# Performance work log

Hardware: AMD Instinct MI355X
Metric: run time of the kernel (lower is better)

## Reference

```python
import jax, jax.numpy as jnp
import numpy as np

# Hyperparameters matching init_kwargs
IN_CH = 64
OUT_CH = 128
KERNEL = (3, 3)
STRIDE = (1, 1)
PADDING = 'SAME'
K_ORDER = 3          # spline order
G_INTERVALS = 3      # grid intervals
GRID_MIN, GRID_MAX = -1.0, 1.0
N_BASIS = G_INTERVALS + K_ORDER  # basis functions per input = 6
PATCH_DIM = IN_CH * KERNEL[0] * KERNEL[1]  # 576


def _grid():
    # Extended uniform knot vector: G + 2k + 1 knots
    h = (GRID_MAX - GRID_MIN) / G_INTERVALS
    return jnp.arange(-K_ORDER, G_INTERVALS + K_ORDER + 1, dtype=jnp.float32) * h + GRID_MIN


def _b_splines(x):
    # x: [N, n_in] -> bases: [N, n_in, G + k]
    grid = _grid()  # [G + 2k + 1]
    xe = x[..., None]  # [N, n_in, 1]
    bases = ((xe >= grid[:-1]) & (xe < grid[1:])).astype(x.dtype)  # order-0, [N, n_in, G+2k]
    for p in range(1, K_ORDER + 1):
        left = (xe - grid[: -(p + 1)]) / (grid[p:-1] - grid[: -(p + 1)]) * bases[..., :-1]
        right = (grid[p + 1:] - xe) / (grid[p + 1:] - grid[1:-p]) * bases[..., 1:]
        bases = left + right
    return bases  # [N, n_in, G + k]


def setup_inputs() -> dict:
    key = jax.random.key(0)
    k0, k1, k2, k3 = jax.random.split(key, 4)
    x = jax.random.normal(k0, (8, 64, 64, IN_CH), dtype=jnp.float32)
    base_w = jax.random.normal(k1, (OUT_CH, PATCH_DIM), dtype=jnp.float32) * 0.05
    spline_w = jax.random.normal(k2, (OUT_CH, PATCH_DIM, N_BASIS), dtype=jnp.float32) * 0.05
    bias = jax.random.normal(k3, (OUT_CH,), dtype=jnp.float32) * 0.05
    return {'x': x, 'base_w': base_w, 'spline_w': spline_w, 'bias': bias}


def reference(x, base_w, spline_w, bias):
    batch = x.shape[0]
    dn = ('NHWC', 'HWIO', 'NHWC')
    patches = jax.lax.conv_general_dilated_patches(
        lhs=x, filter_shape=KERNEL, window_strides=STRIDE, padding=PADDING,
        dimension_numbers=dn)  # [B, H, W, patch_dim]
    out_spatial = patches.shape[1:-1]
    p = patches.reshape(-1, PATCH_DIM)  # [N, patch_dim]
    # EfficientKAN: residual (silu) branch + spline branch + bias
    base_out = jax.nn.silu(p) @ base_w.T                      # [N, out]
    bases = _b_splines(p)                                      # [N, patch_dim, G+k]
    spline_out = jnp.einsum('nig,oig->no', bases, spline_w)    # [N, out]
    y = base_out + spline_out + bias
    return y.reshape(batch, *out_spatial, OUT_CH)
```

## Files before the change

### kernel.cpp

```cpp
#include <hip/hip_runtime.h>

typedef __attribute__((ext_vector_type(8))) short short8;
typedef __attribute__((ext_vector_type(16))) float f32x16;

#define FT2_SHORTS (512u * 4356u * 8u)
#define PLANE16    4356

typedef __attribute__((address_space(3))) unsigned int lds_u32_t;
typedef __attribute__((address_space(1))) const unsigned int g_u32_t;

__device__ __forceinline__ unsigned short f2bf(float x) {
    union { float f; unsigned u; } v; v.f = x;
    unsigned r = v.u + 0x7FFFu + ((v.u >> 16) & 1u);
    return (unsigned short)(r >> 16);
}

__device__ __forceinline__ void feat8(float p, unsigned short* uf) {
    float e   = __expf(-p);
    float sig = 1.f / (1.f + e);
    uf[0] = f2bf(p * sig);
    float u  = p * 1.5f + 4.5f;
    float fj = floorf(u);
    int   j0 = (int)fj;
    float t  = u - fj;
    bool  inr = (u >= 0.f) && (u < 9.f);
    float t2 = t * t, t3 = t2 * t;
    const float c16 = 1.f / 6.f;
    float r0 = t3 * c16;
    float r1 = (-3.f * t3 + 3.f * t2 + 3.f * t + 1.f) * c16;
    float r2 = (3.f * t3 - 6.f * t2 + 4.f) * c16;
    float s1 = 1.f - t;
    float r3 = s1 * s1 * s1 * c16;
#pragma unroll
    for (int g = 0; g < 6; ++g) {
        int r = j0 - g;
        float v = (r == 0) ? r0 : ((r == 1) ? r1 : ((r == 2) ? r2 : ((r == 3) ? r3 : 0.f)));
        uf[1 + g] = f2bf(inr ? v : 0.f);
    }
    uf[7] = 0;
}

__global__ __launch_bounds__(256)
void prep_all(const float* __restrict__ x,
              const float* __restrict__ bw, const float* __restrict__ sw,
              unsigned short* __restrict__ ft, unsigned short* __restrict__ wt) {
    const int blk = blockIdx.x;
    const int tid = threadIdx.x;

    if (tid < 144) {
        int idx = blk * 144 + tid;
        int o = idx / 576;
        int i = idx - o * 576;
        int slab = i >> 3, e = i & 7;
        union { unsigned short u[8]; uint4 v; } pk;
        pk.u[0] = f2bf(bw[o * 576 + i]);
        const float* s = sw + (size_t)(o * 576 + i) * 6;
#pragma unroll
        for (int f = 0; f < 6; ++f) pk.u[1 + f] = f2bf(s[f]);
        pk.u[7] = 0;
        *(uint4*)(wt + ((size_t)slab * 8192 + e * 1024 + o * 8)) = pk.v;
    }

    {
        short8 pad = { 0, 0, (short)0x3CAB, (short)0x3EF5,
                       (short)0x3EF5, (short)0x3CAB, 0, 0 };
        for (int t = tid; t < 260; t += 256) {
            int yy, xx;
            if (t < 66)       { yy = 0;       xx = t; }
            else if (t < 132) { yy = 65;      xx = t - 66; }
            else if (t < 196) { yy = t - 131; xx = 0; }
            else              { yy = t - 195; xx = 65; }
            ((short8*)ft)[blk * PLANE16 + yy * 66 + xx] = pad;
        }
    }

    __shared__ float Xl[64 * 65];
    const int b = blk >> 6, y = blk & 63;
    const float* xl = x + (size_t)blk * 4096;
    for (int f4 = tid; f4 < 1024; f4 += 256) {
        float4 v = ((const float4*)xl)[f4];
        int xx = f4 >> 4, c4 = (f4 & 15) << 2;
        float* d = &Xl[xx * 65 + c4];
        d[0] = v.x; d[1] = v.y; d[2] = v.z; d[3] = v.w;
    }
    __syncthreads();
    const int xx = tid & 63;
    const int cw = tid >> 6;
#pragma unroll 4
    for (int p = 0; p < 16; ++p) {
        int c = cw + (p << 2);
        float pv = Xl[xx * 65 + c];
        union { unsigned short u[8]; uint4 v; } pk;
        feat8(pv, pk.u);
        size_t o16 = (size_t)(c * 8 + b) * PLANE16 + (y + 1) * 66 + (xx + 1);
        *(uint4*)(ft + (o16 << 3)) = pk.v;
    }
}

#define BUF_SHORTS 16384

#define STAGE(sl, q_)                                                                 \
    {                                                                                 \
        unsigned short* bufq = Bufs + (q_) * BUF_SHORTS;                              \
        const unsigned short* bsrc = wt + (size_t)(sl) * 8192;                        \
        _Pragma("unroll")                                                             \
        for (int t = 0; t < 4; ++t) {                                                 \
            int u = wave * 4 + t;                     \
            if (u < 16) {                                                             \
                int boff = u * 512 + lane * 8;                                        \
                __builtin_amdgcn_global_load_lds((g_u32_t*)(bsrc + boff),             \
                                                 (lds_u32_t*)(bufq + boff), 16, 0, 0);\
            } else {                                                                  \
                int ua  = u - 16;                                     \
                int ia  = (sl) * 8 + (ua >> 1);                                       \
                int ln  = ua & 1;                                                     \
                int c_  = (ia * 7282) >> 16;                                          \
                int i9_ = ia - c_ * 9;                                                \
                int kh_ = (i9_ * 11) >> 5;                                            \
                int kw_ = i9_ - kh_ * 3;                                              \
                const unsigned short* asrc = ft +                                     \
                    (((size_t)(c_ * 8 + b) * PLANE16 + (y0 + ln + kh_) * 66 + kw_)    \
                     << 3) + lane * 8;                                                \
                unsigned short* adst = bufq + 8192 + ua * 512 + lane * 8;             \
                __builtin_amdgcn_global_load_lds((g_u32_t*)asrc, (lds_u32_t*)adst,    \
                                                 16, 0, 0);                           \
            }                                                                         \
        }                                                                             \
    }

#define KSTEP(s_)                                                                     \
    {                                                                                 \
        int iloc = 2 * (s_) + h;                                    \
        const unsigned short* Ab = bufr + 8192 + ((iloc << 1) + gl) * 512;            \
        const unsigned short* Bb = bufr + iloc * 1024;                                \
        short8 a0 = *(const short8*)(Ab + (gh * 32 + l32) * 8);                       \
        short8 b0 = *(const short8*)(Bb + (nh * 64 + l32) * 8);                       \
        short8 b1 = *(const short8*)(Bb + (nh * 64 + 32 + l32) * 8);                  \
        acc0 = __builtin_amdgcn_mfma_f32_32x32x16_bf16(a0, b0, acc0, 0, 0, 0);        \
        acc1 = __builtin_amdgcn_mfma_f32_32x32x16_bf16(a0, b1, acc1, 0, 0, 0);        \
    }

#define PHASE(it_, q_, n_, dostage_)                                                  \
    {                                                                                 \
        asm volatile("s_waitcnt vmcnt(" #n_ ")" ::: "memory");                        \
        __builtin_amdgcn_s_barrier();                                                 \
        asm volatile("" ::: "memory");                                                \
        const unsigned short* bufr = Bufs + (q_) * BUF_SHORTS;                        \
        __builtin_amdgcn_s_setprio(1);                                                \
        KSTEP(0) KSTEP(1) KSTEP(2) KSTEP(3)                                           \
        __builtin_amdgcn_s_setprio(0);                                                \
        asm volatile("" ::: "memory");                                                \
        __builtin_amdgcn_s_barrier();                                                 \
        asm volatile("" ::: "memory");                                                \
        if (dostage_) STAGE((it_) + 3, q_);                                           \
    }

__global__ __launch_bounds__(512, 2)
void convkan_gemm(const unsigned short* __restrict__ ft,
                  const unsigned short* __restrict__ wt,
                  const float* __restrict__ bias,
                  float* __restrict__ out) {
    extern __shared__ unsigned short Bufs[];

    const int tid  = threadIdx.x;
    const int mb   = blockIdx.x;
    const int lane = tid & 63;
    const int wave = tid >> 6;
    const int g    = wave >> 1;
    const int nh   = wave & 1;
    const int gl   = g >> 1;
    const int gh   = g & 1;
    const int l32  = lane & 31;
    const int h    = lane >> 5;

    const int b  = mb >> 5;
    const int y0 = (mb & 31) << 1;

    f32x16 acc0, acc1;
#pragma unroll
    for (int e = 0; e < 16; ++e) { acc0[e] = 0.f; acc1[e] = 0.f; }

    STAGE(0, 0);
    STAGE(1, 1);
    STAGE(2, 2);

    for (int it3 = 0; it3 < 23; ++it3) {
        const int it = it3 * 3;
        PHASE(it + 0, 0, 8, true)
        PHASE(it + 1, 1, 8, true)
        PHASE(it + 2, 2, 8, true)
    }
    PHASE(69, 0, 8, false)
    PHASE(70, 1, 4, false)
    PHASE(71, 2, 0, false)

    const int ncol = nh * 64 + l32;
    const float bv0 = bias[ncol];
    const float bv1 = bias[ncol + 32];
    const int prow = mb * 128 + g * 32;
#pragma unroll
    for (int r = 0; r < 16; ++r) {
        int mrow = (r & 3) + ((r >> 2) << 3) + 4 * h;
        float* p = out + (size_t)(prow + mrow) * 128 + ncol;
        p[0]  = acc0[r] + bv0;
        p[32] = acc1[r] + bv1;
    }
}

extern "C" void kernel_launch(void* const* d_in, const int* in_sizes, int n_in,
                              void* d_out, int out_size, void* d_ws, size_t ws_size,
                              hipStream_t stream) {
    (void)in_sizes; (void)n_in; (void)ws_size; (void)out_size;
    const float* x        = (const float*)d_in[0];
    const float* base_w   = (const float*)d_in[1];
    const float* spline_w = (const float*)d_in[2];
    const float* bias     = (const float*)d_in[3];
    float* out = (float*)d_out;

    unsigned short* ft = (unsigned short*)d_ws;
    unsigned short* wt = ft + FT2_SHORTS;

    hipLaunchKernelGGL(prep_all, dim3(512), dim3(256), 0, stream,
                       x, base_w, spline_w, ft, wt);

    const int shmem = 3 * BUF_SHORTS * 2;
    (void)hipFuncSetAttribute((const void*)convkan_gemm,
                              hipFuncAttributeMaxDynamicSharedMemorySize, shmem);
    hipLaunchKernelGGL(convkan_gemm, dim3(256), dim3(512), shmem, stream,
                       ft, wt, bias, out);
}
```

Measured before the change: 140.7 us.

## Split K across 16 waves with 2x2 MFMA tiles and LDS reduction

The GEMM block grows from 512 to 1024 threads. Each wave now owns one K-quarter of every staged slice and computes a 64x64 output tile with four MFMAs. Partial accumulators from the four K-groups are summed through LDS in several barrier-separated rounds before writing output with bias. The aim is more waves to hide latency and fewer LDS reads per MFMA, at the cost of extra reduction traffic, more barriers, and higher register pressure from four accumulators.

```diff
diff --git a/kernel.cpp b/kernel.cpp
--- a/kernel.cpp
+++ b/kernel.cpp
@@ -104,14 +104,14 @@
         unsigned short* bufq = Bufs + (q_) * BUF_SHORTS;                              \
         const unsigned short* bsrc = wt + (size_t)(sl) * 8192;                        \
         _Pragma("unroll")                                                             \
-        for (int t = 0; t < 4; ++t) {                                                 \
-            int u = wave * 4 + t;                     \
+        for (int t = 0; t < 2; ++t) {                                                 \
+            int u = wave * 2 + t;                     \
             if (u < 16) {                                                             \
                 int boff = u * 512 + lane * 8;                                        \
                 __builtin_amdgcn_global_load_lds((g_u32_t*)(bsrc + boff),             \
                                                  (lds_u32_t*)(bufq + boff), 16, 0, 0);\
             } else {                                                                  \
-                int ua  = u - 16;                                     \
+                int ua  = u - 16;                                 \
                 int ia  = (sl) * 8 + (ua >> 1);                                       \
                 int ln  = ua & 1;                                                     \
                 int c_  = (ia * 7282) >> 16;                                          \
@@ -128,34 +128,48 @@
         }                                                                             \
     }
 
-#define KSTEP(s_)                                                                     \
+#define COMPUTE(q_)                                                                   \
     {                                                                                 \
-        int iloc = 2 * (s_) + h;                                    \
-        const unsigned short* Ab = bufr + 8192 + ((iloc << 1) + gl) * 512;            \
-        const unsigned short* Bb = bufr + iloc * 1024;                                \
-        short8 a0 = *(const short8*)(Ab + (gh * 32 + l32) * 8);                       \
-        short8 b0 = *(const short8*)(Bb + (nh * 64 + l32) * 8);                       \
-        short8 b1 = *(const short8*)(Bb + (nh * 64 + 32 + l32) * 8);                  \
-        acc0 = __builtin_amdgcn_mfma_f32_32x32x16_bf16(a0, b0, acc0, 0, 0, 0);        \
-        acc1 = __builtin_amdgcn_mfma_f32_32x32x16_bf16(a0, b1, acc1, 0, 0, 0);        \
-    }
-
-#define PHASE(it_, q_, n_, dostage_)                                                  \
+        const unsigned short* bufr = Bufs + (q_) * BUF_SHORTS;                        \
+        const unsigned short* Ab = bufr + 8192 + ((iloc << 1) + mh) * 512;            \
+        const unsigned short* Bb = bufr + iloc * 1024 + nh * 512;                     \
+        short8 a0 = *(const short8*)(Ab + l32 * 8);                                   \
+        short8 a1 = *(const short8*)(Ab + 256 + l32 * 8);                             \
+        short8 b0 = *(const short8*)(Bb + l32 * 8);                                   \
+        short8 b1 = *(const short8*)(Bb + 256 + l32 * 8);                             \
+        acc00 = __builtin_amdgcn_mfma_f32_32x32x16_bf16(a0, b0, acc00, 0, 0, 0);      \
+        acc01 = __builtin_amdgcn_mfma_f32_32x32x16_bf16(a0, b1, acc01, 0, 0, 0);      \
+        acc10 = __builtin_amdgcn_mfma_f32_32x32x16_bf16(a1, b0, acc10, 0, 0, 0);      \
+        acc11 = __builtin_amdgcn_mfma_f32_32x32x16_bf16(a1, b1, acc11, 0, 0, 0);      \
+    }
+
+#define PHASE(q_, n_, stagesl, dostage_)                                              \
     {                                                                                 \
         asm volatile("s_waitcnt vmcnt(" #n_ ")" ::: "memory");                        \
         __builtin_amdgcn_s_barrier();                                                 \
         asm volatile("" ::: "memory");                                                \
-        const unsigned short* bufr = Bufs + (q_) * BUF_SHORTS;                        \
         __builtin_amdgcn_s_setprio(1);                                                \
-        KSTEP(0) KSTEP(1) KSTEP(2) KSTEP(3)                                           \
+        COMPUTE(q_)                                                                   \
         __builtin_amdgcn_s_setprio(0);                                                \
         asm volatile("" ::: "memory");                                                \
         __builtin_amdgcn_s_barrier();                                                 \
         asm volatile("" ::: "memory");                                                \
-        if (dostage_) STAGE((it_) + 3, q_);                                           \
-    }
-
-__global__ __launch_bounds__(512, 2)
+        if (dostage_) STAGE(stagesl, q_);                                             \
+    }
+
+#define DUMPA(base_, A_)                                                              \
+    {   float4* s4 = (float4*)(red + (base_));                                        \
+        _Pragma("unroll")                                                             \
+        for (int c = 0; c < 4; ++c)                                                   \
+            s4[c * 64 + lane] = make_float4(A_[4*c], A_[4*c+1], A_[4*c+2], A_[4*c+3]); }
+#define ADDA(base_, A_)                                                               \
+    {   const float4* s4 = (const float4*)(red + (base_));                            \
+        _Pragma("unroll")                                                             \
+        for (int c = 0; c < 4; ++c) {                                                 \
+            float4 rv = s4[c * 64 + lane];                                            \
+            A_[4*c] += rv.x; A_[4*c+1] += rv.y; A_[4*c+2] += rv.z; A_[4*c+3] += rv.w; } }
+
+__global__ __launch_bounds__(1024, 4)
 void convkan_gemm(const unsigned short* __restrict__ ft,
                   const unsigned short* __restrict__ wt,
                   const float* __restrict__ bias,
@@ -166,19 +180,19 @@
     const int mb   = blockIdx.x;
     const int lane = tid & 63;
     const int wave = tid >> 6;
-    const int g    = wave >> 1;
+    const int kq   = wave >> 2;
+    const int mh   = (wave >> 1) & 1;
     const int nh   = wave & 1;
-    const int gl   = g >> 1;
-    const int gh   = g & 1;
     const int l32  = lane & 31;
     const int h    = lane >> 5;
+    const int iloc = (kq << 1) + h;
 
     const int b  = mb >> 5;
     const int y0 = (mb & 31) << 1;
 
-    f32x16 acc0, acc1;
-#pragma unroll
-    for (int e = 0; e < 16; ++e) { acc0[e] = 0.f; acc1[e] = 0.f; }
+    f32x16 acc00, acc01, acc10, acc11;
+#pragma unroll
+    for (int e = 0; e < 16; ++e) { acc00[e] = 0.f; acc01[e] = 0.f; acc10[e] = 0.f; acc11[e] = 0.f; }
 
     STAGE(0, 0);
     STAGE(1, 1);
@@ -186,24 +200,51 @@
 
     for (int it3 = 0; it3 < 23; ++it3) {
         const int it = it3 * 3;
-        PHASE(it + 0, 0, 8, true)
-        PHASE(it + 1, 1, 8, true)
-        PHASE(it + 2, 2, 8, true)
-    }
-    PHASE(69, 0, 8, false)
-    PHASE(70, 1, 4, false)
-    PHASE(71, 2, 0, false)
-
-    const int ncol = nh * 64 + l32;
-    const float bv0 = bias[ncol];
-    const float bv1 = bias[ncol + 32];
-    const int prow = mb * 128 + g * 32;
-#pragma unroll
-    for (int r = 0; r < 16; ++r) {
-        int mrow = (r & 3) + ((r >> 2) << 3) + 4 * h;
-        float* p = out + (size_t)(prow + mrow) * 128 + ncol;
-        p[0]  = acc0[r] + bv0;
-        p[32] = acc1[r] + bv1;
+        PHASE(0, 4, it + 3, true)
+        PHASE(1, 4, it + 4, true)
+        PHASE(2, 4, it + 5, true)
+    }
+    PHASE(0, 4, 0, false)
+    PHASE(1, 2, 0, false)
+    PHASE(2, 0, 0, false)
+
+    __syncthreads();
+    float* red = (float*)Bufs;
+    const int grp = mh * 2 + nh;
+
+    if (kq >= 2) { DUMPA(((grp << 1) + (kq - 2)) * 2048,        acc00);
+                   DUMPA(((grp << 1) + (kq - 2)) * 2048 + 1024, acc01); }
+    __syncthreads();
+    if (kq < 2)  { ADDA(((grp << 1) + kq) * 2048,        acc00);
+                   ADDA(((grp << 1) + kq) * 2048 + 1024, acc01); }
+    __syncthreads();
+    if (kq >= 2) { DUMPA(((grp << 1) + (kq - 2)) * 2048,        acc10);
+                   DUMPA(((grp << 1) + (kq - 2)) * 2048 + 1024, acc11); }
+    __syncthreads();
+    if (kq < 2)  { ADDA(((grp << 1) + kq) * 2048,        acc10);
+                   ADDA(((grp << 1) + kq) * 2048 + 1024, acc11); }
+    __syncthreads();
+    if (kq == 1) { DUMPA(grp * 4096,        acc00); DUMPA(grp * 4096 + 1024, acc01);
+                   DUMPA(grp * 4096 + 2048, acc10); DUMPA(grp * 4096 + 3072, acc11); }
+    __syncthreads();
+    if (kq == 0) {
+        ADDA(grp * 4096,        acc00); ADDA(grp * 4096 + 1024, acc01);
+        ADDA(grp * 4096 + 2048, acc10); ADDA(grp * 4096 + 3072, acc11);
+
+        const int ncol = nh * 64 + l32;
+        const float bv0 = bias[ncol];
+        const float bv1 = bias[ncol + 32];
+        const int prow = mb * 128 + mh * 64;
+#pragma unroll
+        for (int r = 0; r < 16; ++r) {
+            int mrow = (r & 3) + ((r >> 2) << 3) + 4 * h;
+            float* p = out + (size_t)(prow + mrow) * 128 + ncol;
+            p[0]  = acc00[r] + bv0;
+            p[32] = acc01[r] + bv1;
+            float* p2 = out + (size_t)(prow + 32 + mrow) * 128 + ncol;
+            p2[0]  = acc10[r] + bv0;
+            p2[32] = acc11[r] + bv1;
+        }
     }
 }
 
@@ -226,6 +267,6 @@
     const int shmem = 3 * BUF_SHORTS * 2;
     (void)hipFuncSetAttribute((const void*)convkan_gemm,
                               hipFuncAttributeMaxDynamicSharedMemorySize, shmem);
-    hipLaunchKernelGGL(convkan_gemm, dim3(256), dim3(512), shmem, stream,
+    hipLaunchKernelGGL(convkan_gemm, dim3(256), dim3(1024), shmem, stream,
                        ft, wt, bias, out);
 }
```

Measured after the change: 133.4 us. 1.05x faster.
